# Performance work log

Measured on AMD Instinct MI355X. Metric: run time of the kernel, lower is better.

## Reference

```python
import jax, jax.numpy as jnp
import numpy as np

TAU = 1.0
NUM_CLASSES = 14
LOSS_WEIGHT = 1.0
KSUM = 27.0  # sum of the 3x3x3 all-ones kernel


def setup_inputs() -> dict:
    key = jax.random.key(0)
    k1, k2, k3 = jax.random.split(key, 3)
    shape = (2, 14, 96, 96, 96)
    return {
        "preds_S": jax.random.normal(k1, shape, dtype=jnp.float32),
        "preds_T": jax.random.normal(k2, shape, dtype=jnp.float32),
        "outputs_T": jax.random.normal(k3, shape, dtype=jnp.float32),
    }


def _boundaries(targets):
    # targets: [B, H, W, D] int class map. For each class, boundary voxels are
    # those where the 3x3x3 box-sum of the one-hot mask is in (0, 27):
    # conv==27 (fully interior) is zeroed, conv>0 is set to 1.
    onehot = jax.nn.one_hot(targets, NUM_CLASSES, axis=1, dtype=jnp.float32)  # [B,K,H,W,D]
    box = jax.lax.reduce_window(
        onehot, 0.0, jax.lax.add,
        window_dimensions=(1, 1, 3, 3, 3),
        window_strides=(1, 1, 1, 1, 1),
        padding=((0, 0), (0, 0), (1, 1), (1, 1), (1, 1)),
    )
    return jnp.where((box > 0) & (box != KSUM), 1.0, 0.0)  # [B,K,H,W,D]


def reference(preds_S, preds_T, outputs_T):
    B, C = preds_S.shape[:2]
    targets = jnp.argmax(outputs_T, axis=1)  # [B,H,W,D] (detached in original)
    boundary = _boundaries(targets).reshape(B, NUM_CLASSES, -1)  # [B,K,V]

    sS = preds_S.reshape(B, C, -1) / TAU
    sT = preds_T.reshape(B, C, -1) / TAU
    log_s = jax.nn.log_softmax(sS, axis=1)   # softmax over class dim (dim=0 of [C,V] view)
    log_t = jax.nn.log_softmax(sT, axis=1)
    t = jnp.exp(log_t)
    # pointwise KL summed over classes per voxel: [B,V]
    pk = jnp.sum(t * (log_t - log_s), axis=1)

    n = jnp.sum(boundary, axis=-1)                      # [B,K] boundary voxel counts
    num = jnp.einsum('bkv,bv->bk', boundary, pk)        # KL mass on boundary voxels
    # KLDivLoss(reduction='mean') divides by numel = C * n; skip empty boundaries
    term = jnp.where(n > 0, num / (C * jnp.maximum(n, 1.0)), 0.0)
    return LOSS_WEIGHT * (TAU ** 2) * jnp.sum(term)
```

## Files before the change

### kernel.cpp

```cpp
#include <hip/hip_runtime.h>

#define NC 14
#define DIM 96
#define NV (DIM*DIM*DIM)
#define WS 104
#define HS (104*98)
#define PADV2 (104*98*98)
#define SLABB ((size_t)PADV2*2*2)

__global__ void __launch_bounds__(256)
argmax_bit_kernel(const float* __restrict__ outT, unsigned short* __restrict__ bm) {
    int tid = blockIdx.x * 256 + threadIdx.x;
    if (tid >= 2 * (NV / 4)) return;
    int b = tid >= (NV / 4);
    int q = tid - b * (NV / 4);
    int v4 = q * 4;
    const float* p = outT + (size_t)b * NC * NV + v4;
    float4 best = *(const float4*)p;
    int bx = 0, by = 0, bz = 0, bw = 0;
#pragma unroll
    for (int c = 1; c < NC; ++c) {
        float4 val = *(const float4*)(p + (size_t)c * NV);
        if (val.x > best.x) { best.x = val.x; bx = c; }
        if (val.y > best.y) { best.y = val.y; by = c; }
        if (val.z > best.z) { best.z = val.z; bz = c; }
        if (val.w > best.w) { best.w = val.w; bw = c; }
    }
    int d = v4 % DIM;
    int t1 = v4 / DIM;
    int w = t1 % DIM;
    int h = t1 / DIM;
    ushort4 out;
    out.x = (unsigned short)(1u << bx);
    out.y = (unsigned short)(1u << by);
    out.z = (unsigned short)(1u << bz);
    out.w = (unsigned short)(1u << bw);
    *(ushort4*)(bm + (size_t)b * PADV2 + (h + 1) * HS + (w + 1) * WS + (d + 4)) = out;
}

__global__ void or_d_kernel(const unsigned short* __restrict__ bm,
                            unsigned short* __restrict__ dm) {
    int p = blockIdx.x * blockDim.x + threadIdx.x;
    if (p >= 2 * PADV2) return;
    int pd = (p % PADV2) % WS;
    if (pd < 4 || pd > 99) return;
    dm[p] = (unsigned short)(bm[p - 1] | bm[p] | bm[p + 1]);
}

__global__ void or_w_kernel(const unsigned short* __restrict__ dm,
                            unsigned short* __restrict__ wm) {
    int p = blockIdx.x * blockDim.x + threadIdx.x;
    if (p >= 2 * PADV2) return;
    int pw = ((p % PADV2) / WS) % 98;
    if (pw < 1 || pw > 96) return;
    wm[p] = (unsigned short)(dm[p - WS] | dm[p] | dm[p + WS]);
}

__global__ void __launch_bounds__(256)
boundary_kl_kernel(const float* __restrict__ pS, const float* __restrict__ pT,
                   const unsigned short* __restrict__ wm,
                   float* __restrict__ acc_num, float* __restrict__ acc_cnt) {
    const int b = blockIdx.x & 1;
    const int bslot = blockIdx.x >> 1;
    int tid4 = bslot * 256 + threadIdx.x;
    int v4 = tid4 * 4;
    int d = v4 % DIM;
    int t1 = v4 / DIM;
    int w = t1 % DIM;
    int h = t1 / DIM;

    const float* sS = pS + (size_t)b * NC * NV + v4;
    const float* sT = pT + (size_t)b * NC * NV + v4;
    const unsigned short* w0 = wm + (size_t)b * PADV2;

    int off = (h + 1) * HS + (w + 1) * WS + (d + 4);
    ushort4 m0 = *(const ushort4*)(w0 + off - HS);
    ushort4 m1 = *(const ushort4*)(w0 + off);
    ushort4 m2 = *(const ushort4*)(w0 + off + HS);

    float4 seS = {0.f, 0.f, 0.f, 0.f};
    float4 seT = {0.f, 0.f, 0.f, 0.f};
    float4 dot = {0.f, 0.f, 0.f, 0.f};
#pragma unroll
    for (int c = 0; c < NC; ++c) {
        float4 vs = *(const float4*)(sS + (size_t)c * NV);
        float4 vt = *(const float4*)(sT + (size_t)c * NV);
        float e;
        seS.x += __expf(vs.x); e = __expf(vt.x); seT.x += e; dot.x += e * (vt.x - vs.x);
        seS.y += __expf(vs.y); e = __expf(vt.y); seT.y += e; dot.y += e * (vt.y - vs.y);
        seS.z += __expf(vs.z); e = __expf(vt.z); seT.z += e; dot.z += e * (vt.z - vs.z);
        seS.w += __expf(vs.w); e = __expf(vt.w); seT.w += e; dot.w += e * (vt.w - vs.w);
    }
    float pk[4];
    pk[0] = dot.x / seT.x + __logf(seS.x) - __logf(seT.x);
    pk[1] = dot.y / seT.y + __logf(seS.y) - __logf(seT.y);
    pk[2] = dot.z / seT.z + __logf(seS.z) - __logf(seT.z);
    pk[3] = dot.w / seT.w + __logf(seS.w) - __logf(seT.w);

    unsigned mk[4];
    mk[0] = (unsigned)(m0.x | m1.x | m2.x);
    mk[1] = (unsigned)(m0.y | m1.y | m2.y);
    mk[2] = (unsigned)(m0.z | m1.z | m2.z);
    mk[3] = (unsigned)(m0.w | m1.w | m2.w);

    bool hwint = ((unsigned)(h - 1) <= 93u) && ((unsigned)(w - 1) <= 93u);
    float num[NC], cnt[NC];
#pragma unroll
    for (int c = 0; c < NC; ++c) { num[c] = 0.f; cnt[c] = 0.f; }
#pragma unroll
    for (int j = 0; j < 4; ++j) {
        bool interior = hwint && ((unsigned)(d + j - 1) <= 93u);
        unsigned m = mk[j];
        if (interior && (m & (m - 1)) == 0u) m = 0u;
        float p = pk[j];
#pragma unroll
        for (int c = 0; c < NC; ++c) {
            float hit = (float)((m >> c) & 1u);
            num[c] = fmaf(hit, p, num[c]);
            cnt[c] += hit;
        }
    }

    __shared__ float snum[NC], scnt[NC];
    if (threadIdx.x < NC) { snum[threadIdx.x] = 0.f; scnt[threadIdx.x] = 0.f; }
    __syncthreads();
    int lane = threadIdx.x & 63;
#pragma unroll
    for (int c = 0; c < NC; ++c) {
        float s = num[c], n = cnt[c];
#pragma unroll
        for (int o = 32; o; o >>= 1) {
            s += __shfl_xor(s, o);
            n += __shfl_xor(n, o);
        }
        if (lane == 0) {
            atomicAdd(&snum[c], s);
            atomicAdd(&scnt[c], n);
        }
    }
    __syncthreads();
    if (threadIdx.x < NC) {
        atomicAdd(&acc_num[b * NC + threadIdx.x], snum[threadIdx.x]);
        atomicAdd(&acc_cnt[b * NC + threadIdx.x], scnt[threadIdx.x]);
    }
}

__global__ void finalize_kernel(const float* __restrict__ acc_num,
                                const float* __restrict__ acc_cnt,
                                float* __restrict__ out) {
    if (threadIdx.x == 0 && blockIdx.x == 0) {
        float s = 0.f;
        for (int i = 0; i < 2 * NC; ++i) {
            float n = acc_cnt[i];
            if (n > 0.f) s += acc_num[i] / ((float)NC * n);
        }
        out[0] = s;
    }
}

extern "C" void kernel_launch(void* const* d_in, const int* in_sizes, int n_in,
                              void* d_out, int out_size, void* d_ws, size_t ws_size,
                              hipStream_t stream) {
    const float* preds_S = (const float*)d_in[0];
    const float* preds_T = (const float*)d_in[1];
    const float* outputs_T = (const float*)d_in[2];

    char* ws = (char*)d_ws;
    float* acc_num = (float*)ws;
    float* acc_cnt = acc_num + 32;
    unsigned short* bm = (unsigned short*)(ws + 256);
    unsigned short* dm = (unsigned short*)(ws + 256 + SLABB);
    unsigned short* wm = (unsigned short*)(ws + 256 + 2 * SLABB);

    hipMemsetAsync(d_ws, 0, 256 + 3 * SLABB, stream);

    {
        int threadsTotal = 2 * (NV / 4);
        argmax_bit_kernel<<<(threadsTotal + 255) / 256, 256, 0, stream>>>(outputs_T, bm);
    }
    {
        int total = 2 * PADV2;
        int blocks = (total + 255) / 256;
        or_d_kernel<<<blocks, 256, 0, stream>>>(bm, dm);
        or_w_kernel<<<blocks, 256, 0, stream>>>(dm, wm);
    }
    {
        boundary_kl_kernel<<<1728, 256, 0, stream>>>(preds_S, preds_T, wm,
                                                     acc_num, acc_cnt);
    }
    finalize_kernel<<<1, 64, 0, stream>>>(acc_num, acc_cnt, (float*)d_out);
}
```

Measured before the change: 94.24 us.

## Widen all boundary-KL kernels to 8 voxels per thread and shrink workspace memset

Each thread now handles 8 voxels. The padded mask row stride grows to 112 so 16-byte uint4 loads and stores line up. The two OR-dilation passes now work on 8-element chunks with vector loads instead of scalar ushorts. Only the argmax bitmask slab and the accumulators are zeroed; the dilation buffers are no longer memset, since every location later read is assumed to be written first. Accumulators are spread 64 bytes apart to cut atomic contention, at the cost of more registers per thread and more reliance on the padding being exactly right.

```diff
diff --git a/kernel.cpp b/kernel.cpp
--- a/kernel.cpp
+++ b/kernel.cpp
@@ -3,115 +3,159 @@
 #define NC 14
 #define DIM 96
 #define NV (DIM*DIM*DIM)
-#define WS 104
-#define HS (104*98)
-#define PADV2 (104*98*98)
-#define SLABB ((size_t)PADV2*2*2)
-
-__global__ void __launch_bounds__(256)
+#define NV8 (NV/8)
+#define WS2 112
+#define HS2 (112*98)
+#define PADV (112*98*98)
+#define SLABB ((size_t)PADV*2*2)
+
+__global__ void __launch_bounds__(128)
 argmax_bit_kernel(const float* __restrict__ outT, unsigned short* __restrict__ bm) {
-    int tid = blockIdx.x * 256 + threadIdx.x;
-    if (tid >= 2 * (NV / 4)) return;
-    int b = tid >= (NV / 4);
-    int q = tid - b * (NV / 4);
-    int v4 = q * 4;
-    const float* p = outT + (size_t)b * NC * NV + v4;
-    float4 best = *(const float4*)p;
-    int bx = 0, by = 0, bz = 0, bw = 0;
+    int tid = blockIdx.x * 128 + threadIdx.x;
+    int b = tid >= NV8;
+    int q = tid - b * NV8;
+    int v8 = q * 8;
+    const float* p = outT + (size_t)b * NC * NV + v8;
+    float4 a0 = *(const float4*)p;
+    float4 a1 = *(const float4*)(p + 4);
+    float bv[8] = {a0.x, a0.y, a0.z, a0.w, a1.x, a1.y, a1.z, a1.w};
+    int bi[8] = {0, 0, 0, 0, 0, 0, 0, 0};
 #pragma unroll
     for (int c = 1; c < NC; ++c) {
-        float4 val = *(const float4*)(p + (size_t)c * NV);
-        if (val.x > best.x) { best.x = val.x; bx = c; }
-        if (val.y > best.y) { best.y = val.y; by = c; }
-        if (val.z > best.z) { best.z = val.z; bz = c; }
-        if (val.w > best.w) { best.w = val.w; bw = c; }
-    }
-    int d = v4 % DIM;
-    int t1 = v4 / DIM;
+        float4 v0 = *(const float4*)(p + (size_t)c * NV);
+        float4 v1 = *(const float4*)(p + (size_t)c * NV + 4);
+        float vv[8] = {v0.x, v0.y, v0.z, v0.w, v1.x, v1.y, v1.z, v1.w};
+#pragma unroll
+        for (int j = 0; j < 8; ++j)
+            if (vv[j] > bv[j]) { bv[j] = vv[j]; bi[j] = c; }
+    }
+    int d = v8 % DIM;
+    int t1 = v8 / DIM;
     int w = t1 % DIM;
     int h = t1 / DIM;
-    ushort4 out;
-    out.x = (unsigned short)(1u << bx);
-    out.y = (unsigned short)(1u << by);
-    out.z = (unsigned short)(1u << bz);
-    out.w = (unsigned short)(1u << bw);
-    *(ushort4*)(bm + (size_t)b * PADV2 + (h + 1) * HS + (w + 1) * WS + (d + 4)) = out;
-}
-
-__global__ void or_d_kernel(const unsigned short* __restrict__ bm,
-                            unsigned short* __restrict__ dm) {
-    int p = blockIdx.x * blockDim.x + threadIdx.x;
-    if (p >= 2 * PADV2) return;
-    int pd = (p % PADV2) % WS;
-    if (pd < 4 || pd > 99) return;
-    dm[p] = (unsigned short)(bm[p - 1] | bm[p] | bm[p + 1]);
-}
-
-__global__ void or_w_kernel(const unsigned short* __restrict__ dm,
-                            unsigned short* __restrict__ wm) {
-    int p = blockIdx.x * blockDim.x + threadIdx.x;
-    if (p >= 2 * PADV2) return;
-    int pw = ((p % PADV2) / WS) % 98;
+    uint4 out;
+    out.x = (1u << bi[0]) | ((1u << bi[1]) << 16);
+    out.y = (1u << bi[2]) | ((1u << bi[3]) << 16);
+    out.z = (1u << bi[4]) | ((1u << bi[5]) << 16);
+    out.w = (1u << bi[6]) | ((1u << bi[7]) << 16);
+    *(uint4*)(bm + (size_t)b * PADV + (h + 1) * HS2 + (w + 1) * WS2 + (d + 8)) = out;
+}
+
+__global__ void __launch_bounds__(256)
+or_d_kernel(const unsigned short* __restrict__ bm, unsigned short* __restrict__ dm) {
+    int idx = blockIdx.x * 256 + threadIdx.x;
+    if (idx >= 2 * PADV / 8) return;
+    int base = idx * 8;
+    int pd0 = base % WS2;
+    if (pd0 == 0 || pd0 == 104) return;
+    uint4 X = *(const uint4*)(bm + base);
+    unsigned short xm1 = bm[base - 1];
+    unsigned short xp8 = bm[base + 8];
+    unsigned x[10];
+    x[0] = xm1;
+    x[1] = X.x & 0xFFFFu; x[2] = X.x >> 16;
+    x[3] = X.y & 0xFFFFu; x[4] = X.y >> 16;
+    x[5] = X.z & 0xFFFFu; x[6] = X.z >> 16;
+    x[7] = X.w & 0xFFFFu; x[8] = X.w >> 16;
+    x[9] = xp8;
+    unsigned r[8];
+#pragma unroll
+    for (int j = 0; j < 8; ++j) r[j] = x[j] | x[j + 1] | x[j + 2];
+    uint4 out;
+    out.x = r[0] | (r[1] << 16);
+    out.y = r[2] | (r[3] << 16);
+    out.z = r[4] | (r[5] << 16);
+    out.w = r[6] | (r[7] << 16);
+    *(uint4*)(dm + base) = out;
+}
+
+__global__ void __launch_bounds__(256)
+or_w_kernel(const unsigned short* __restrict__ dm, unsigned short* __restrict__ wm) {
+    int idx = blockIdx.x * 256 + threadIdx.x;
+    if (idx >= 2 * PADV / 8) return;
+    int base = idx * 8;
+    int pw = ((base % PADV) / WS2) % 98;
     if (pw < 1 || pw > 96) return;
-    wm[p] = (unsigned short)(dm[p - WS] | dm[p] | dm[p + WS]);
-}
-
-__global__ void __launch_bounds__(256)
+    uint4 a = *(const uint4*)(dm + base - WS2);
+    uint4 c = *(const uint4*)(dm + base);
+    uint4 e = *(const uint4*)(dm + base + WS2);
+    uint4 out;
+    out.x = a.x | c.x | e.x;
+    out.y = a.y | c.y | e.y;
+    out.z = a.z | c.z | e.z;
+    out.w = a.w | c.w | e.w;
+    *(uint4*)(wm + base) = out;
+}
+
+__global__ void __launch_bounds__(128)
 boundary_kl_kernel(const float* __restrict__ pS, const float* __restrict__ pT,
                    const unsigned short* __restrict__ wm,
-                   float* __restrict__ acc_num, float* __restrict__ acc_cnt) {
+                   float* __restrict__ acc) {
     const int b = blockIdx.x & 1;
-    const int bslot = blockIdx.x >> 1;
-    int tid4 = bslot * 256 + threadIdx.x;
-    int v4 = tid4 * 4;
-    int d = v4 % DIM;
-    int t1 = v4 / DIM;
+    int tid8 = (blockIdx.x >> 1) * 128 + threadIdx.x;
+    int v8 = tid8 * 8;
+    int d = v8 % DIM;
+    int t1 = v8 / DIM;
     int w = t1 % DIM;
     int h = t1 / DIM;
 
-    const float* sS = pS + (size_t)b * NC * NV + v4;
-    const float* sT = pT + (size_t)b * NC * NV + v4;
-    const unsigned short* w0 = wm + (size_t)b * PADV2;
-
-    int off = (h + 1) * HS + (w + 1) * WS + (d + 4);
-    ushort4 m0 = *(const ushort4*)(w0 + off - HS);
-    ushort4 m1 = *(const ushort4*)(w0 + off);
-    ushort4 m2 = *(const ushort4*)(w0 + off + HS);
-
-    float4 seS = {0.f, 0.f, 0.f, 0.f};
-    float4 seT = {0.f, 0.f, 0.f, 0.f};
-    float4 dot = {0.f, 0.f, 0.f, 0.f};
+    const float* sS = pS + (size_t)b * NC * NV + v8;
+    const float* sT = pT + (size_t)b * NC * NV + v8;
+    const unsigned short* w0 = wm + (size_t)b * PADV;
+
+    int off = (h + 1) * HS2 + (w + 1) * WS2 + (d + 8);
+    uint4 M0 = *(const uint4*)(w0 + off - HS2);
+    uint4 M1 = *(const uint4*)(w0 + off);
+    uint4 M2 = *(const uint4*)(w0 + off + HS2);
+    uint4 MM;
+    MM.x = M0.x | M1.x | M2.x;
+    MM.y = M0.y | M1.y | M2.y;
+    MM.z = M0.z | M1.z | M2.z;
+    MM.w = M0.w | M1.w | M2.w;
+    unsigned mk[8];
+    mk[0] = MM.x & 0xFFFFu; mk[1] = MM.x >> 16;
+    mk[2] = MM.y & 0xFFFFu; mk[3] = MM.y >> 16;
+    mk[4] = MM.z & 0xFFFFu; mk[5] = MM.z >> 16;
+    mk[6] = MM.w & 0xFFFFu; mk[7] = MM.w >> 16;
+
+    float4 seSA = {0,0,0,0}, seTA = {0,0,0,0}, dotA = {0,0,0,0};
+    float4 seSB = {0,0,0,0}, seTB = {0,0,0,0}, dotB = {0,0,0,0};
 #pragma unroll
     for (int c = 0; c < NC; ++c) {
-        float4 vs = *(const float4*)(sS + (size_t)c * NV);
-        float4 vt = *(const float4*)(sT + (size_t)c * NV);
+        const float* a = sS + (size_t)c * NV;
+        const float* t = sT + (size_t)c * NV;
+        float4 vsA = *(const float4*)a;
+        float4 vsB = *(const float4*)(a + 4);
+        float4 vtA = *(const float4*)t;
+        float4 vtB = *(const float4*)(t + 4);
         float e;
-        seS.x += __expf(vs.x); e = __expf(vt.x); seT.x += e; dot.x += e * (vt.x - vs.x);
-        seS.y += __expf(vs.y); e = __expf(vt.y); seT.y += e; dot.y += e * (vt.y - vs.y);
-        seS.z += __expf(vs.z); e = __expf(vt.z); seT.z += e; dot.z += e * (vt.z - vs.z);
-        seS.w += __expf(vs.w); e = __expf(vt.w); seT.w += e; dot.w += e * (vt.w - vs.w);
-    }
-    float pk[4];
-    pk[0] = dot.x / seT.x + __logf(seS.x) - __logf(seT.x);
-    pk[1] = dot.y / seT.y + __logf(seS.y) - __logf(seT.y);
-    pk[2] = dot.z / seT.z + __logf(seS.z) - __logf(seT.z);
-    pk[3] = dot.w / seT.w + __logf(seS.w) - __logf(seT.w);
-
-    unsigned mk[4];
-    mk[0] = (unsigned)(m0.x | m1.x | m2.x);
-    mk[1] = (unsigned)(m0.y | m1.y | m2.y);
-    mk[2] = (unsigned)(m0.z | m1.z | m2.z);
-    mk[3] = (unsigned)(m0.w | m1.w | m2.w);
+        seSA.x += __expf(vsA.x); e = __expf(vtA.x); seTA.x += e; dotA.x += e * (vtA.x - vsA.x);
+        seSA.y += __expf(vsA.y); e = __expf(vtA.y); seTA.y += e; dotA.y += e * (vtA.y - vsA.y);
+        seSA.z += __expf(vsA.z); e = __expf(vtA.z); seTA.z += e; dotA.z += e * (vtA.z - vsA.z);
+        seSA.w += __expf(vsA.w); e = __expf(vtA.w); seTA.w += e; dotA.w += e * (vtA.w - vsA.w);
+        seSB.x += __expf(vsB.x); e = __expf(vtB.x); seTB.x += e; dotB.x += e * (vtB.x - vsB.x);
+        seSB.y += __expf(vsB.y); e = __expf(vtB.y); seTB.y += e; dotB.y += e * (vtB.y - vsB.y);
+        seSB.z += __expf(vsB.z); e = __expf(vtB.z); seTB.z += e; dotB.z += e * (vtB.z - vsB.z);
+        seSB.w += __expf(vsB.w); e = __expf(vtB.w); seTB.w += e; dotB.w += e * (vtB.w - vsB.w);
+    }
+    float pk[8];
+    pk[0] = dotA.x / seTA.x + __logf(seSA.x) - __logf(seTA.x);
+    pk[1] = dotA.y / seTA.y + __logf(seSA.y) - __logf(seTA.y);
+    pk[2] = dotA.z / seTA.z + __logf(seSA.z) - __logf(seTA.z);
+    pk[3] = dotA.w / seTA.w + __logf(seSA.w) - __logf(seTA.w);
+    pk[4] = dotB.x / seTB.x + __logf(seSB.x) - __logf(seTB.x);
+    pk[5] = dotB.y / seTB.y + __logf(seSB.y) - __logf(seTB.y);
+    pk[6] = dotB.z / seTB.z + __logf(seSB.z) - __logf(seTB.z);
+    pk[7] = dotB.w / seTB.w + __logf(seSB.w) - __logf(seTB.w);
 
     bool hwint = ((unsigned)(h - 1) <= 93u) && ((unsigned)(w - 1) <= 93u);
     float num[NC], cnt[NC];
 #pragma unroll
     for (int c = 0; c < NC; ++c) { num[c] = 0.f; cnt[c] = 0.f; }
 #pragma unroll
-    for (int j = 0; j < 4; ++j) {
-        bool interior = hwint && ((unsigned)(d + j - 1) <= 93u);
+    for (int j = 0; j < 8; ++j) {
         unsigned m = mk[j];
-        if (interior && (m & (m - 1)) == 0u) m = 0u;
+        if (hwint && ((unsigned)(d + j - 1) <= 93u) && (m & (m - 1)) == 0u) m = 0u;
         float p = pk[j];
 #pragma unroll
         for (int c = 0; c < NC; ++c) {
@@ -140,19 +184,17 @@
     }
     __syncthreads();
     if (threadIdx.x < NC) {
-        atomicAdd(&acc_num[b * NC + threadIdx.x], snum[threadIdx.x]);
-        atomicAdd(&acc_cnt[b * NC + threadIdx.x], scnt[threadIdx.x]);
-    }
-}
-
-__global__ void finalize_kernel(const float* __restrict__ acc_num,
-                                const float* __restrict__ acc_cnt,
-                                float* __restrict__ out) {
+        atomicAdd(&acc[(b * NC + threadIdx.x) * 16], snum[threadIdx.x]);
+        atomicAdd(&acc[(32 + b * NC + threadIdx.x) * 16], scnt[threadIdx.x]);
+    }
+}
+
+__global__ void finalize_kernel(const float* __restrict__ acc, float* __restrict__ out) {
     if (threadIdx.x == 0 && blockIdx.x == 0) {
         float s = 0.f;
         for (int i = 0; i < 2 * NC; ++i) {
-            float n = acc_cnt[i];
-            if (n > 0.f) s += acc_num[i] / ((float)NC * n);
+            float n = acc[(32 + i) * 16];
+            if (n > 0.f) s += acc[i * 16] / ((float)NC * n);
         }
         out[0] = s;
     }
@@ -166,27 +208,20 @@
     const float* outputs_T = (const float*)d_in[2];
 
     char* ws = (char*)d_ws;
-    float* acc_num = (float*)ws;
-    float* acc_cnt = acc_num + 32;
-    unsigned short* bm = (unsigned short*)(ws + 256);
-    unsigned short* dm = (unsigned short*)(ws + 256 + SLABB);
-    unsigned short* wm = (unsigned short*)(ws + 256 + 2 * SLABB);
-
-    hipMemsetAsync(d_ws, 0, 256 + 3 * SLABB, stream);
-
+    float* acc = (float*)ws;
+    unsigned short* bm = (unsigned short*)(ws + 4096);
+    unsigned short* dm = (unsigned short*)(ws + 4096 + SLABB);
+    unsigned short* wm = (unsigned short*)(ws + 4096 + 2 * SLABB);
+
+    hipMemsetAsync(d_ws, 0, 4096 + SLABB, stream);
+
+    argmax_bit_kernel<<<(2 * NV8) / 128, 128, 0, stream>>>(outputs_T, bm);
     {
-        int threadsTotal = 2 * (NV / 4);
-        argmax_bit_kernel<<<(threadsTotal + 255) / 256, 256, 0, stream>>>(outputs_T, bm);
-    }
-    {
-        int total = 2 * PADV2;
-        int blocks = (total + 255) / 256;
+        int chunks = 2 * PADV / 8;
+        int blocks = (chunks + 255) / 256;
         or_d_kernel<<<blocks, 256, 0, stream>>>(bm, dm);
         or_w_kernel<<<blocks, 256, 0, stream>>>(dm, wm);
     }
-    {
-        boundary_kl_kernel<<<1728, 256, 0, stream>>>(preds_S, preds_T, wm,
-                                                     acc_num, acc_cnt);
-    }
-    finalize_kernel<<<1, 64, 0, stream>>>(acc_num, acc_cnt, (float*)d_out);
-}
+    boundary_kl_kernel<<<2 * (NV8 / 128), 128, 0, stream>>>(preds_S, preds_T, wm, acc);
+    finalize_kernel<<<1, 64, 0, stream>>>(acc, (float*)d_out);
+}
```

Measured after the change: 96.79 us. 1.03x slower.
